# Optimization experiments

Measured on AMD Instinct MI355X. Metric: run time of the kernel, lower is better.

## Reference

```python
import jax, jax.numpy as jnp
import numpy as np

# Model constants (from init_kwargs)
B, S, D = 2, 2048, 2048          # batch, seq, d_model
E = 64                           # num_routed_experts
TOP_K = 4
BOT = int(D * 0.25)              # bottle_dim = 512
EXP = 1536                       # routed expert hidden (bigmac_expert_size)
DFF = 8192                       # shared expert hidden (d_ff)
Z_LOSS_W = 1e-4
MOE_SCALE = 0.5                  # 1/(1 + [num_shared_experts>0])


def setup_inputs() -> dict:
    key = jax.random.key(0)
    ks = jax.random.split(key, 10)
    std = 0.011
    return {
        "x": jax.random.normal(ks[0], (B, S, D), jnp.float32),
        "router_w": jax.random.normal(ks[1], (E, D), jnp.float32) * 0.02,
        "gate_w": jax.random.normal(ks[2], (DFF, D), jnp.float32) * std,
        "up_w": jax.random.normal(ks[3], (DFF, D), jnp.float32) * std,
        "down_w": jax.random.normal(ks[4], (D, DFF), jnp.float32) * std,
        "w_down": jax.random.normal(ks[5], (BOT, D), jnp.float32) * std,
        "w_up": jax.random.normal(ks[6], (D, BOT), jnp.float32) * std,
        "w12": jax.random.normal(ks[7], (E, BOT, 2 * EXP), jnp.float32) * std,
        "w3": jax.random.normal(ks[8], (E, EXP, BOT), jnp.float32) * std,
    }


def reference(x, router_w, gate_w, up_w, down_w, w_down, w_up, w12, w3):
    b, s, d = x.shape
    h = x.reshape(-1, d)                       # [N, D]
    N = h.shape[0]
    NT = N * TOP_K                             # total routed token-slots

    # ---- router (fp32) ----
    logits = h @ router_w.T                    # [N, E]
    scores = jax.nn.sigmoid(logits)
    z_loss = jnp.mean(jnp.nan_to_num(logits) ** 2) * Z_LOSS_W
    # expert_bias is None -> selection_scores == scores
    _, topk_idx = jax.lax.top_k(scores, TOP_K)             # [N, K]
    topk_logits = jnp.take_along_axis(logits, topk_idx, axis=1)
    gating = jax.nn.softmax(topk_logits, axis=-1)          # [N, K]

    # ---- shared expert (SwiGLU) ----
    shared = (jax.nn.silu(h @ gate_w.T) * (h @ up_w.T)) @ down_w.T  # [N, D]

    # ---- bottleneck down-projection ----
    down = h @ w_down.T                        # [N, BOT]

    # ---- dispatch: sort tokens by expert, capacity-limited padding ----
    flat = topk_idx.reshape(-1)                # [NT]
    order = jnp.argsort(flat)                  # stable sort
    sorted_e = flat[order]
    counts = jax.ops.segment_sum(jnp.ones(NT, jnp.int32), flat, num_segments=E)
    ptr = jnp.cumsum(counts) - counts          # expert start offsets
    local = jnp.arange(NT) - ptr[sorted_e]     # rank within expert
    max_load = (NT // E // 8 + 6) * 8          # capacity per expert
    num_slots = E * max_load
    mask = local < max_load
    slots = sorted_e * max_load + local
    token_idx = jnp.repeat(jnp.arange(N), TOP_K)

    # reverse_map[slot] = source token row (N = dummy row); extra slot absorbs dropped tokens
    rev = jnp.full(num_slots + 1, N, dtype=jnp.int32)
    rev = rev.at[jnp.where(mask, slots, num_slots)].set(token_idx[order].astype(jnp.int32))
    rev = rev[:num_slots]

    h_dummy = jnp.concatenate([down, jnp.zeros((1, BOT), down.dtype)], axis=0)
    padding = h_dummy[rev].reshape(E, max_load, BOT)

    # ---- grouped expert GEMMs ----
    h12 = jnp.einsum('eld,edf->elf', padding, w12)   # [E, max_load, 2*EXP]
    h1, h2 = jnp.split(h12, 2, axis=-1)
    po = jnp.einsum('elf,efd->eld', jax.nn.silu(h1) * h2, w3)  # [E, max_load, BOT]
    po = jnp.concatenate([po.reshape(-1, BOT), jnp.zeros((1, BOT), po.dtype)], axis=0)

    # ---- combine: gather back, weight by gating ----
    gm = jnp.full(NT, num_slots, dtype=jnp.int32)
    gm = gm.at[order].set(jnp.where(mask, slots, num_slots).astype(jnp.int32))
    gathered = po[gm].reshape(N, TOP_K, BOT)
    routed = jnp.einsum('nk,nkd->nd', gating, gathered) @ w_up.T  # [N, D]

    # eval mode: route_scale = 1.0, aux_loss = 0
    out = ((shared + routed) * MOE_SCALE).reshape(b, s, d)
    return out, z_loss
```

## Files before the change

### kernel.cpp

```cpp
#include <hip/hip_runtime.h>

#define DEV __device__ __forceinline__

typedef __attribute__((ext_vector_type(4))) float f4;
typedef __attribute__((ext_vector_type(8))) __bf16 bfrag;
typedef __attribute__((ext_vector_type(4))) unsigned short us4;
typedef __attribute__((ext_vector_type(8))) unsigned short us8;

#define NTOK   4096
#define DMODEL 2048
#define NEXP   64
#define MAXLD  304
#define NSLOT  19456

DEV unsigned short f2bf(float f){
  union { float f; unsigned int i; } u; u.f = f;
  unsigned int r = u.i + 0x7fffu + ((u.i >> 16) & 1u);
  return (unsigned short)(r >> 16);
}
DEV float bf2f(unsigned short b){
  union { unsigned int i; float f; } u; u.i = ((unsigned int)b) << 16;
  return u.f;
}

DEV void gl_lds16(const unsigned short* g, unsigned short* l){
  __builtin_amdgcn_global_load_lds(
      (const __attribute__((address_space(1))) void*)g,
      (__attribute__((address_space(3))) void*)l, 16, 0, 0);
}

template<int EPI>
__global__ __launch_bounds__(256) void gemm_bt(
    const unsigned short* __restrict__ A, const unsigned short* __restrict__ B,
    void* __restrict__ Cp, const float* __restrict__ addin,
    int M, int N, int K, long long sA, long long sB, long long sC)
{
  __shared__ unsigned short As[128*32];
  __shared__ unsigned short Bs[128*32];
  A += (long long)blockIdx.z * sA;
  B += (long long)blockIdx.z * sB;
  const long long cbase = (long long)blockIdx.z * sC;
  const int bm = blockIdx.y * 128, bn = blockIdx.x * 128;
  const int t = threadIdx.x, wave = t >> 6, lane = t & 63;
  const int wm = (wave >> 1) * 64, wn = (wave & 1) * 64;
  const int fr = lane & 15, kg = lane >> 4;

  f4 acc[4][4];
#pragma unroll
  for (int m = 0; m < 4; ++m)
#pragma unroll
    for (int n = 0; n < 4; ++n)
      acc[m][n] = f4{0.f, 0.f, 0.f, 0.f};

  const int i0 = t, i1 = 256 + t;
  int ar0 = bm + (i0 >> 2); if (ar0 > M - 1) ar0 = M - 1;
  int ar1 = bm + (i1 >> 2); if (ar1 > M - 1) ar1 = M - 1;
  int br0 = bn + (i0 >> 2); if (br0 > N - 1) br0 = N - 1;
  int br1 = bn + (i1 >> 2); if (br1 > N - 1) br1 = N - 1;
  const unsigned short* ap0 = A + (long long)ar0 * K + (i0 & 3) * 8;
  const unsigned short* ap1 = A + (long long)ar1 * K + (i1 & 3) * 8;
  const unsigned short* bp0 = B + (long long)br0 * K + (i0 & 3) * 8;
  const unsigned short* bp1 = B + (long long)br1 * K + (i1 & 3) * 8;
  unsigned short* da0 = As + wave * 512;
  unsigned short* da1 = As + 2048 + wave * 512;
  unsigned short* db0 = Bs + wave * 512;
  unsigned short* db1 = Bs + 2048 + wave * 512;

  for (int k0 = 0; k0 < K; k0 += 32){
    gl_lds16(ap0, da0);
    gl_lds16(ap1, da1);
    gl_lds16(bp0, db0);
    gl_lds16(bp1, db1);
    ap0 += 32; ap1 += 32; bp0 += 32; bp1 += 32;
    __syncthreads();
    bfrag af[4], bfv[4];
#pragma unroll
    for (int m = 0; m < 4; ++m) af[m] = *(const bfrag*)&As[(wm + m*16 + fr)*32 + kg*8];
#pragma unroll
    for (int n = 0; n < 4; ++n) bfv[n] = *(const bfrag*)&Bs[(wn + n*16 + fr)*32 + kg*8];
#pragma unroll
    for (int m = 0; m < 4; ++m)
#pragma unroll
      for (int n = 0; n < 4; ++n)
        acc[m][n] = __builtin_amdgcn_mfma_f32_16x16x32_bf16(af[m], bfv[n], acc[m][n], 0, 0, 0);
    __syncthreads();
  }

#pragma unroll
  for (int m = 0; m < 4; ++m){
    const int row0 = bm + wm + m*16 + kg*4;
#pragma unroll
    for (int n = 0; n < 4; ++n){
      const int col = bn + wn + n*16 + fr;
      if (col < N){
        f4 v = acc[m][n];
#pragma unroll
        for (int r = 0; r < 4; ++r){
          const int row = row0 + r;
          if (row < M){
            const long long off = cbase + (long long)row * N + col;
            if (EPI == 0)      ((unsigned short*)Cp)[off] = f2bf(v[r]);
            else if (EPI == 1) ((float*)Cp)[off] = v[r];
            else               ((float*)Cp)[off] = (v[r] + addin[off]) * 0.5f;
          }
        }
      }
    }
  }
}

__global__ void cvt_bf16(const float* __restrict__ in, unsigned short* __restrict__ out,
                         long long n4)
{
  long long i = (long long)blockIdx.x * 256 + threadIdx.x;
  if (i >= n4) return;
  float4 v = ((const float4*)in)[i];
  us4 o; o[0] = f2bf(v.x); o[1] = f2bf(v.y); o[2] = f2bf(v.z); o[3] = f2bf(v.w);
  ((us4*)out)[i] = o;
}

__global__ __launch_bounds__(256) void transpose_cvt(const float* __restrict__ in,
    unsigned short* __restrict__ out, int R, int C)
{
  __shared__ float tile[32][33];
  const long long z = blockIdx.z;
  const float* ip = in + z * (long long)R * C;
  unsigned short* op = out + z * (long long)R * C;
  const int r0 = blockIdx.y * 32, c0 = blockIdx.x * 32;
  const int t = threadIdx.x;
  const int lr = t >> 3, lc = (t & 7) * 4;
  float4 v = *(const float4*)(ip + (long long)(r0 + lr) * C + c0 + lc);
  tile[lr][lc+0] = v.x; tile[lr][lc+1] = v.y; tile[lr][lc+2] = v.z; tile[lr][lc+3] = v.w;
  __syncthreads();
  const int oc = t >> 3, orr = (t & 7) * 4;
  us4 o;
  o[0] = f2bf(tile[orr+0][oc]); o[1] = f2bf(tile[orr+1][oc]);
  o[2] = f2bf(tile[orr+2][oc]); o[3] = f2bf(tile[orr+3][oc]);
  *(us4*)(op + (long long)(c0 + oc) * R + r0 + orr) = o;
}

__global__ void router_topk(const float* __restrict__ logits, int* __restrict__ topk,
                            float* __restrict__ gating, float* __restrict__ zout)
{
  const int t = threadIdx.x, w = t >> 6, lane = t & 63;
  const int n = blockIdx.x * 4 + w;
  const float lg = logits[(long long)n * 64 + lane];
  float z = lg * lg;
#pragma unroll
  for (int off = 32; off; off >>= 1) z += __shfl_xor(z, off);
  __shared__ float zs[4];
  if (lane == 0) zs[w] = z;
  __syncthreads();
  if (t == 0) atomicAdd(zout, (zs[0]+zs[1]+zs[2]+zs[3]) * (0.0001f / 262144.0f));

  float cur = lg;
  float tl[4]; int ti[4];
#pragma unroll
  for (int k = 0; k < 4; ++k){
    float s = cur; int si = lane;
#pragma unroll
    for (int off = 32; off; off >>= 1){
      float so = __shfl_xor(s, off); int io = __shfl_xor(si, off);
      if (so > s || (so == s && io < si)){ s = so; si = io; }
    }
    tl[k] = s; ti[k] = si;
    if (lane == si) cur = -3.0e38f;
  }
  if (lane == 0){
    const float m0 = tl[0];
    const float e0 = __expf(tl[0]-m0), e1 = __expf(tl[1]-m0),
                e2 = __expf(tl[2]-m0), e3 = __expf(tl[3]-m0);
    const float inv = 1.0f / (e0 + e1 + e2 + e3);
    topk[n*4+0] = ti[0]; topk[n*4+1] = ti[1]; topk[n*4+2] = ti[2]; topk[n*4+3] = ti[3];
    gating[n*4+0] = e0*inv; gating[n*4+1] = e1*inv; gating[n*4+2] = e2*inv; gating[n*4+3] = e3*inv;
  }
}

__global__ void scan_route(const int* __restrict__ topk, int* __restrict__ gm,
                           int* __restrict__ rev, int* __restrict__ counts)
{
  const int e = blockIdx.x;
  const int t = threadIdx.x, w = t >> 6, lane = t & 63;
  __shared__ int wtot[4];
  int running = 0;
  for (int c = 0; c < 16384; c += 256){
    const int j = c + t;
    const bool p = (topk[j] == e);
    const unsigned long long m = __ballot(p);
    const int prefix = __popcll(m & ((1ull << lane) - 1ull));
    if (lane == 0) wtot[w] = __popcll(m);
    __syncthreads();
    int woff = 0;
#pragma unroll
    for (int i = 0; i < 4; ++i){ if (i < w) woff += wtot[i]; }
    const int btot = wtot[0] + wtot[1] + wtot[2] + wtot[3];
    if (p){
      const int rank = running + woff + prefix;
      gm[j] = (rank < MAXLD) ? (e * MAXLD + rank) : NSLOT;
      if (rank < MAXLD) rev[e * MAXLD + rank] = j >> 2;
    }
    running += btot;
    __syncthreads();
  }
  if (t == 0) counts[e] = running;
}

__global__ void gather_pad(const unsigned short* __restrict__ down, const int* __restrict__ rev,
                           const int* __restrict__ counts, unsigned short* __restrict__ pad)
{
  const int idx = blockIdx.x * 256 + threadIdx.x;
  const int s = idx >> 6, c8 = (idx & 63) * 8;
  const int e = s / MAXLD;
  const int r = s - e * MAXLD;
  int cnt = counts[e]; if (cnt > MAXLD) cnt = MAXLD;
  us8 v = {0,0,0,0,0,0,0,0};
  if (r < cnt){
    const int tok = rev[s];
    v = *(const us8*)(down + (long long)tok * 512 + c8);
  }
  *(us8*)(pad + (long long)s * 512 + c8) = v;
}

__global__ void silu_mul(const unsigned short* __restrict__ G, const unsigned short* __restrict__ U,
                         unsigned short* __restrict__ O, long long ldg, long long ldu, long long ldo,
                         long long cols8, long long total)
{
  const long long idx = (long long)blockIdx.x * 256 + threadIdx.x;
  if (idx >= total) return;
  const long long rr = idx / cols8;
  const long long cc = (idx - rr * cols8) * 8;
  us8 g = *(const us8*)(G + rr * ldg + cc);
  us8 u = *(const us8*)(U + rr * ldu + cc);
  us8 o;
#pragma unroll
  for (int j = 0; j < 8; ++j){
    const float gf = bf2f(g[j]);
    const float s = gf / (1.0f + __expf(-gf));
    o[j] = f2bf(s * bf2f(u[j]));
  }
  *(us8*)(O + rr * ldo + cc) = o;
}

__global__ void combine_moe(const unsigned short* __restrict__ po, const int* __restrict__ gm,
                            const float* __restrict__ gating, unsigned short* __restrict__ routed)
{
  const int idx = blockIdx.x * 256 + threadIdx.x;
  const int n = idx >> 6, c8 = (idx & 63) * 8;
  float acc[8] = {0,0,0,0,0,0,0,0};
#pragma unroll
  for (int k = 0; k < 4; ++k){
    const int slot = gm[n*4 + k];
    if (slot < NSLOT){
      const float gw = gating[n*4 + k];
      us8 v = *(const us8*)(po + (long long)slot * 512 + c8);
#pragma unroll
      for (int j = 0; j < 8; ++j) acc[j] += gw * bf2f(v[j]);
    }
  }
  us8 o;
#pragma unroll
  for (int j = 0; j < 8; ++j) o[j] = f2bf(acc[j]);
  *(us8*)(routed + (long long)n * 512 + c8) = o;
}

extern "C" void kernel_launch(void* const* d_in, const int* in_sizes, int n_in,
                              void* d_out, int out_size, void* d_ws, size_t ws_size,
                              hipStream_t stream)
{
  const float* x      = (const float*)d_in[0];
  const float* rw     = (const float*)d_in[1];
  const float* gate_w = (const float*)d_in[2];
  const float* up_w   = (const float*)d_in[3];
  const float* down_w = (const float*)d_in[4];
  const float* w_down = (const float*)d_in[5];
  const float* w_up   = (const float*)d_in[6];
  const float* w12    = (const float*)d_in[7];
  const float* w3     = (const float*)d_in[8];
  float* out = (float*)d_out;

  char* ws = (char*)d_ws;
  unsigned short* HBF   = (unsigned short*)(ws + 0ull);
  unsigned short* RWBF  = (unsigned short*)(ws + 16777216ull);
  unsigned short* GATEB = (unsigned short*)(ws + 17039360ull);
  unsigned short* UPB   = (unsigned short*)(ws + 50593792ull);
  unsigned short* DWB   = (unsigned short*)(ws + 84148224ull);
  unsigned short* WDB   = (unsigned short*)(ws + 117702656ull);
  unsigned short* WUB   = (unsigned short*)(ws + 119799808ull);
  unsigned short* W12T  = (unsigned short*)(ws + 121896960ull);
  unsigned short* W3T   = (unsigned short*)(ws + 323223552ull);
  float*          LOGIT = (float*)(ws + 423886848ull);
  int*            TOPKI = (int*)(ws + 424935424ull);
  float*          GATE4 = (float*)(ws + 425000960ull);
  int*            GM    = (int*)(ws + 425066496ull);
  int*            CNT   = (int*)(ws + 425132032ull);
  int*            REV   = (int*)(ws + 425132288ull);
  unsigned short* GU    = (unsigned short*)(ws + 425210112ull);
  unsigned short* ACTS  = (unsigned short*)(ws + 559427840ull);
  float*          SHRD  = (float*)(ws + 626536704ull);
  unsigned short* DNB   = (unsigned short*)(ws + 660091136ull);
  unsigned short* PAD   = (unsigned short*)(ws + 664285440ull);
  unsigned short* PO    = (unsigned short*)(ws + 684208384ull);
  unsigned short* RTD   = (unsigned short*)(ws + 704131328ull);

  hipMemsetAsync((char*)d_out + 8388608ull * 4, 0, 4, stream);

  cvt_bf16<<<8192,  256, 0, stream>>>(x,      HBF,   2097152);
  cvt_bf16<<<128,   256, 0, stream>>>(rw,     RWBF,  32768);
  cvt_bf16<<<16384, 256, 0, stream>>>(gate_w, GATEB, 4194304);
  cvt_bf16<<<16384, 256, 0, stream>>>(up_w,   UPB,   4194304);
  cvt_bf16<<<16384, 256, 0, stream>>>(down_w, DWB,   4194304);
  cvt_bf16<<<1024,  256, 0, stream>>>(w_down, WDB,   262144);
  cvt_bf16<<<1024,  256, 0, stream>>>(w_up,   WUB,   262144);
  transpose_cvt<<<dim3(96,16,64), 256, 0, stream>>>(w12, W12T, 512, 3072);
  transpose_cvt<<<dim3(16,48,64), 256, 0, stream>>>(w3,  W3T,  1536, 512);

  gemm_bt<1><<<dim3(1,32,1), 256, 0, stream>>>(HBF, RWBF, LOGIT, nullptr,
                                               4096, 64, 2048, 0, 0, 0);
  router_topk<<<1024, 256, 0, stream>>>(LOGIT, TOPKI, GATE4, out + 8388608);
  scan_route<<<64, 256, 0, stream>>>(TOPKI, GM, REV, CNT);

  gemm_bt<0><<<dim3(64,32,1), 256, 0, stream>>>(HBF, GATEB, GU, nullptr,
                                                4096, 8192, 2048, 0, 0, 0);
  gemm_bt<0><<<dim3(64,32,1), 256, 0, stream>>>(HBF, UPB, GU + 33554432ull, nullptr,
                                                4096, 8192, 2048, 0, 0, 0);
  silu_mul<<<16384, 256, 0, stream>>>(GU, GU + 33554432ull, ACTS, 8192, 8192, 8192,
                                      1024, 4194304);
  gemm_bt<1><<<dim3(16,32,1), 256, 0, stream>>>(ACTS, DWB, SHRD, nullptr,
                                                4096, 2048, 8192, 0, 0, 0);

  gemm_bt<0><<<dim3(4,32,1), 256, 0, stream>>>(HBF, WDB, DNB, nullptr,
                                               4096, 512, 2048, 0, 0, 0);
  gather_pad<<<4864, 256, 0, stream>>>(DNB, REV, CNT, PAD);
  gemm_bt<0><<<dim3(24,3,64), 256, 0, stream>>>(PAD, W12T, GU, nullptr,
                                                304, 3072, 512, 155648, 1572864, 933888);
  silu_mul<<<14592, 256, 0, stream>>>(GU, GU + 1536, ACTS, 3072, 3072, 1536,
                                      192, 3735552);
  gemm_bt<0><<<dim3(4,3,64), 256, 0, stream>>>(ACTS, W3T, PO, nullptr,
                                               304, 512, 1536, 466944, 786432, 155648);
  combine_moe<<<1024, 256, 0, stream>>>(PO, GM, GATE4, RTD);

  gemm_bt<2><<<dim3(16,32,1), 256, 0, stream>>>(RTD, WUB, out, SHRD,
                                                4096, 2048, 512, 0, 0, 0);
}
```

Measured before the change: 1.346 ms.

## Add large-tile 512-thread pipelined GEMM for shared-expert and output GEMMs

Adds a new GEMM kernel with 256x256 or 128x256 tiles, 8 waves, BK=64, double-buffered LDS with XOR swizzle and staged direct global-to-LDS loads interleaved with MFMA phases under raised scheduling priority. A workgroup ID remap groups blocks to improve L2 reuse. It replaces the 128x128 GEMM for the shared-expert gate/up/down projections and the final w_up projection, aiming for higher arithmetic intensity and better latency hiding. It relies on the dimensions dividing the tiles exactly and on carefully hand-tuned waitcnt counts, which could be fragile.

```diff
diff --git a/kernel.cpp b/kernel.cpp
--- a/kernel.cpp
+++ b/kernel.cpp
@@ -27,6 +27,174 @@
   __builtin_amdgcn_global_load_lds(
       (const __attribute__((address_space(1))) void*)g,
       (__attribute__((address_space(3))) void*)l, 16, 0, 0);
+}
+
+template<int BM, int EPI>
+__global__ __launch_bounds__(512, 1) void gemm2(
+    const unsigned short* __restrict__ A, const unsigned short* __restrict__ B,
+    void* __restrict__ Cp, const float* __restrict__ addin, int M, int N, int K)
+{
+  constexpr int ALD = BM / 128;
+  constexpr int MQ  = BM / 64;
+  constexpr int HR  = BM / 2;
+  __shared__ unsigned short As[2][2][HR * 64];
+  __shared__ unsigned short Bs[2][2][128 * 64];
+
+  const int nwg = gridDim.x * gridDim.y;
+  int bid = blockIdx.y * gridDim.x + blockIdx.x;
+  bid = (bid & 7) * (nwg >> 3) + (bid >> 3);
+  const int bx = bid % gridDim.x, by = bid / gridDim.x;
+  const int bm = by * BM, bn = bx * 256;
+
+  const int t = threadIdx.x, lane = t & 63, wave = t >> 6;
+  const int ha = wave >> 2;
+  const int wn = (wave & 3) * 64;
+  const int hb = wn >> 7;
+  const int cb = wn & 127;
+  const int fr = lane & 15, kg = lane >> 4;
+
+  const int r0 = t >> 3;
+  const int s0 = (t & 7) ^ (r0 & 7);
+
+#define STG_AH(d_, h_, s_) do {                                                          \
+    gl_lds16(A + (long long)(bm + (h_) * HR + r0) * K + (long long)(s_) * 64 + s0 * 8,   \
+             &As[d_][h_][(wave * 64) * 8]);                                              \
+    if (ALD == 2)                                                                        \
+      gl_lds16(A + (long long)(bm + (h_) * HR + r0 + 64) * K + (long long)(s_) * 64 + s0 * 8, \
+               &As[d_][h_][(512 + wave * 64) * 8]);                                      \
+  } while (0)
+#define STG_BH(d_, h_, s_) do {                                                          \
+    gl_lds16(B + (long long)(bn + (h_) * 128 + r0) * K + (long long)(s_) * 64 + s0 * 8,  \
+             &Bs[d_][h_][(wave * 64) * 8]);                                              \
+    gl_lds16(B + (long long)(bn + (h_) * 128 + r0 + 64) * K + (long long)(s_) * 64 + s0 * 8, \
+             &Bs[d_][h_][(512 + wave * 64) * 8]);                                        \
+  } while (0)
+
+  f4 acc[2 * MQ][4];
+#pragma unroll
+  for (int m = 0; m < 2 * MQ; ++m)
+#pragma unroll
+    for (int n = 0; n < 4; ++n) acc[m][n] = f4{0.f, 0.f, 0.f, 0.f};
+
+  const int ns = K >> 6;
+
+  STG_BH(0, 0, 0); STG_AH(0, 0, 0); STG_BH(0, 1, 0); STG_AH(0, 1, 0);
+  STG_BH(1, 0, 1); STG_AH(1, 0, 1);
+  asm volatile("s_waitcnt vmcnt(%0)" :: "i"(2 + ALD) : "memory");
+  __builtin_amdgcn_s_barrier();
+
+  for (int tt = 0; tt < ns; ++tt){
+    const int d = tt & 1, nd = d ^ 1;
+    bfrag af[MQ][2], bf[2][2][2];
+
+#pragma unroll
+    for (int ni = 0; ni < 2; ++ni)
+#pragma unroll
+      for (int kh = 0; kh < 2; ++kh){
+        const int cn = cb + ni * 16 + fr;
+        bf[0][ni][kh] = *(const bfrag*)&Bs[d][hb][cn * 64 + ((((kh << 2) | kg) ^ (cn & 7)) << 3)];
+      }
+#pragma unroll
+    for (int mi = 0; mi < MQ; ++mi)
+#pragma unroll
+      for (int kh = 0; kh < 2; ++kh){
+        const int rh = mi * 16 + fr;
+        af[mi][kh] = *(const bfrag*)&As[d][ha][rh * 64 + ((((kh << 2) | kg) ^ (rh & 7)) << 3)];
+      }
+    if (tt + 1 < ns) STG_BH(nd, 1, tt + 1);
+    if constexpr (BM == 256) asm volatile("s_waitcnt lgkmcnt(8)");
+    else                     asm volatile("s_waitcnt lgkmcnt(4)");
+    __builtin_amdgcn_s_barrier();
+    asm volatile("s_waitcnt lgkmcnt(0)");
+    __builtin_amdgcn_s_setprio(1);
+#pragma unroll
+    for (int mi = 0; mi < MQ; ++mi)
+#pragma unroll
+      for (int ni = 0; ni < 2; ++ni)
+#pragma unroll
+        for (int kh = 0; kh < 2; ++kh)
+          acc[mi][ni] = __builtin_amdgcn_mfma_f32_16x16x32_bf16(af[mi][kh], bf[0][ni][kh], acc[mi][ni], 0, 0, 0);
+    __builtin_amdgcn_s_setprio(0);
+    __builtin_amdgcn_s_barrier();
+
+#pragma unroll
+    for (int ni = 0; ni < 2; ++ni)
+#pragma unroll
+      for (int kh = 0; kh < 2; ++kh){
+        const int cn = cb + 32 + ni * 16 + fr;
+        bf[1][ni][kh] = *(const bfrag*)&Bs[d][hb][cn * 64 + ((((kh << 2) | kg) ^ (cn & 7)) << 3)];
+      }
+    if (tt + 1 < ns) STG_AH(nd, 1, tt + 1);
+    __builtin_amdgcn_s_barrier();
+    asm volatile("s_waitcnt lgkmcnt(0)");
+    __builtin_amdgcn_s_setprio(1);
+#pragma unroll
+    for (int mi = 0; mi < MQ; ++mi)
+#pragma unroll
+      for (int ni = 0; ni < 2; ++ni)
+#pragma unroll
+        for (int kh = 0; kh < 2; ++kh)
+          acc[mi][2 + ni] = __builtin_amdgcn_mfma_f32_16x16x32_bf16(af[mi][kh], bf[1][ni][kh], acc[mi][2 + ni], 0, 0, 0);
+    __builtin_amdgcn_s_setprio(0);
+    __builtin_amdgcn_s_barrier();
+
+#pragma unroll
+    for (int mi = 0; mi < MQ; ++mi)
+#pragma unroll
+      for (int kh = 0; kh < 2; ++kh){
+        const int rh = MQ * 16 + mi * 16 + fr;
+        af[mi][kh] = *(const bfrag*)&As[d][ha][rh * 64 + ((((kh << 2) | kg) ^ (rh & 7)) << 3)];
+      }
+    if (tt + 2 < ns) STG_BH(d, 0, tt + 2);
+    __builtin_amdgcn_s_barrier();
+    asm volatile("s_waitcnt lgkmcnt(0)");
+    __builtin_amdgcn_s_setprio(1);
+#pragma unroll
+    for (int mi = 0; mi < MQ; ++mi)
+#pragma unroll
+      for (int ni = 0; ni < 2; ++ni)
+#pragma unroll
+        for (int kh = 0; kh < 2; ++kh)
+          acc[MQ + mi][2 + ni] = __builtin_amdgcn_mfma_f32_16x16x32_bf16(af[mi][kh], bf[1][ni][kh], acc[MQ + mi][2 + ni], 0, 0, 0);
+    __builtin_amdgcn_s_setprio(0);
+    __builtin_amdgcn_s_barrier();
+
+    if (tt + 2 < ns) STG_AH(d, 0, tt + 2);
+    __builtin_amdgcn_s_barrier();
+    __builtin_amdgcn_s_setprio(1);
+#pragma unroll
+    for (int mi = 0; mi < MQ; ++mi)
+#pragma unroll
+      for (int ni = 0; ni < 2; ++ni)
+#pragma unroll
+        for (int kh = 0; kh < 2; ++kh)
+          acc[MQ + mi][ni] = __builtin_amdgcn_mfma_f32_16x16x32_bf16(af[mi][kh], bf[0][ni][kh], acc[MQ + mi][ni], 0, 0, 0);
+    __builtin_amdgcn_s_setprio(0);
+    if (tt + 2 < ns)      asm volatile("s_waitcnt vmcnt(%0)" :: "i"(2 + ALD) : "memory");
+    else if (tt + 1 < ns) asm volatile("s_waitcnt vmcnt(0)" ::: "memory");
+    if (tt + 1 < ns) __builtin_amdgcn_s_barrier();
+  }
+
+#pragma unroll
+  for (int mh = 0; mh < 2; ++mh)
+#pragma unroll
+    for (int mi = 0; mi < MQ; ++mi){
+      const int row0 = bm + ha * HR + mh * (HR / 2) + mi * 16 + kg * 4;
+#pragma unroll
+      for (int nf = 0; nf < 4; ++nf){
+        const int col = bn + wn + nf * 16 + fr;
+        f4 v = acc[mh * MQ + mi][nf];
+#pragma unroll
+        for (int r = 0; r < 4; ++r){
+          const long long off = (long long)(row0 + r) * N + col;
+          if (EPI == 0)      ((unsigned short*)Cp)[off] = f2bf(v[r]);
+          else if (EPI == 1) ((float*)Cp)[off] = v[r];
+          else               ((float*)Cp)[off] = (v[r] + addin[off]) * 0.5f;
+        }
+      }
+    }
+#undef STG_AH
+#undef STG_BH
 }
 
 template<int EPI>
@@ -319,14 +487,11 @@
   router_topk<<<1024, 256, 0, stream>>>(LOGIT, TOPKI, GATE4, out + 8388608);
   scan_route<<<64, 256, 0, stream>>>(TOPKI, GM, REV, CNT);
 
-  gemm_bt<0><<<dim3(64,32,1), 256, 0, stream>>>(HBF, GATEB, GU, nullptr,
-                                                4096, 8192, 2048, 0, 0, 0);
-  gemm_bt<0><<<dim3(64,32,1), 256, 0, stream>>>(HBF, UPB, GU + 33554432ull, nullptr,
-                                                4096, 8192, 2048, 0, 0, 0);
+  gemm2<256,0><<<dim3(32,16), 512, 0, stream>>>(HBF, GATEB, GU, nullptr, 4096, 8192, 2048);
+  gemm2<256,0><<<dim3(32,16), 512, 0, stream>>>(HBF, UPB, GU + 33554432ull, nullptr, 4096, 8192, 2048);
   silu_mul<<<16384, 256, 0, stream>>>(GU, GU + 33554432ull, ACTS, 8192, 8192, 8192,
                                       1024, 4194304);
-  gemm_bt<1><<<dim3(16,32,1), 256, 0, stream>>>(ACTS, DWB, SHRD, nullptr,
-                                                4096, 2048, 8192, 0, 0, 0);
+  gemm2<128,1><<<dim3(8,32), 512, 0, stream>>>(ACTS, DWB, SHRD, nullptr, 4096, 2048, 8192);
 
   gemm_bt<0><<<dim3(4,32,1), 256, 0, stream>>>(HBF, WDB, DNB, nullptr,
                                                4096, 512, 2048, 0, 0, 0);
@@ -339,6 +504,5 @@
                                                304, 512, 1536, 466944, 786432, 155648);
   combine_moe<<<1024, 256, 0, stream>>>(PO, GM, GATE4, RTD);
 
-  gemm_bt<2><<<dim3(16,32,1), 256, 0, stream>>>(RTD, WUB, out, SHRD,
-                                                4096, 2048, 512, 0, 0, 0);
-}
+  gemm2<128,2><<<dim3(8,32), 512, 0, stream>>>(RTD, WUB, out, SHRD, 4096, 2048, 512);
+}
```

Result: faster. 1.209 ms (-10.2%).
